# Performance work log

Measured on AMD Instinct MI355X. Metric: run time of the kernel, lower is better.

Reference implementation:

```python
import jax, jax.numpy as jnp
import numpy as np

QMIN, QMAX = -128, 127  # 8-bit signed quantized range


def setup_inputs() -> dict:
    key = jax.random.key(0)
    k0, k1, k2, k3 = jax.random.split(key, 4)
    N, Cin, H, W = 64, 128, 56, 56
    Cout, K = 128, 3
    x = jax.random.randint(k0, (N, Cin, H, W), -128, 128, dtype=jnp.int32).astype(jnp.int8)
    weight = jax.random.randint(k1, (Cout, Cin, K, K), -128, 128, dtype=jnp.int32).astype(jnp.int8)
    # int32 bias (already shifted by -Zx*sum(W) in the original quantization flow)
    bias = jax.random.randint(k2, (Cout,), -4096, 4096, dtype=jnp.int32)
    input_scale = jnp.float32(0.02)
    weight_scale = jax.random.uniform(k3, (Cout,), minval=0.001, maxval=0.01, dtype=jnp.float32)  # per-channel
    output_scale = jnp.float32(0.05)
    input_zero_point = -3   # python int, constant
    output_zero_point = -2  # python int, constant
    return {"x": x, "weight": weight, "bias": bias,
            "input_scale": input_scale, "weight_scale": weight_scale,
            "output_scale": output_scale,
            "input_zero_point": input_zero_point,
            "output_zero_point": output_zero_point}


def reference(x, weight, bias, input_scale, weight_scale, output_scale,
              input_zero_point, output_zero_point):
    # pad spatial dims with the INPUT zero point (padding=(1,1), as in the torch module)
    xp = jnp.pad(x, ((0, 0), (0, 0), (1, 1), (1, 1)), constant_values=input_zero_point)
    acc = jax.lax.conv_general_dilated(
        xp.astype(jnp.int32), weight.astype(jnp.int32),
        window_strides=(1, 1), padding='VALID',
        rhs_dilation=(1, 1), dimension_numbers=('NCHW', 'OIHW', 'NCHW'))
    acc = acc + bias[None, :, None, None]                       # [N,Co,Ho,Wo] int32
    # requantize: per-output-channel scale, shift by output zero point
    scale = (input_scale * weight_scale / output_scale)[None, :, None, None]
    out = acc.astype(jnp.float32) * scale + jnp.float32(output_zero_point)
    return jnp.clip(jnp.round(out), QMIN, QMAX).astype(jnp.int8)
```

## Files before the change

### kernel.cpp

```cpp
#include <hip/hip_runtime.h>


#define CIN  128
#define COUT 128
#define HW   56
#define NPIX (HW * HW)
#define ROWS  4
#define QROWS 6
#define QCOLS 58
#define NQ (QROWS * QCOLS)

typedef int v4i  __attribute__((ext_vector_type(4)));
typedef int v16i __attribute__((ext_vector_type(16)));

__global__ __launch_bounds__(256) void pack_w2(const int* __restrict__ w_g,
                                               unsigned* __restrict__ wp2) {
    int i = blockIdx.x * 256 + threadIdx.x;
    if (i >= 36 * 128 * 8) return;
    int dw   = i & 7;
    int cout = (i >> 3) & 127;
    int step = i >> 10;
    int t  = step >> 2;
    int cb = step & 3;
    unsigned d = 0;
#pragma unroll
    for (int b = 0; b < 4; ++b) {
        int ci = cb * 32 + dw * 4 + b;
        int v = w_g[(cout * CIN + ci) * 9 + t];
        d |= (unsigned)(v & 0xFF) << (8 * b);
    }
    int g  = (cout << 1) | (dw >> 2);
    int gs = g ^ ((g >> 3) & 7);
    wp2[step * 1024 + gs * 4 + (dw & 3)] = d;
}

__global__ __launch_bounds__(256, 2) void conv_mfma(
    const int* __restrict__ x_g, const int* __restrict__ wp2,
    const int* __restrict__ bias, const float* __restrict__ in_s,
    const float* __restrict__ w_s, const float* __restrict__ out_s,
    const int* __restrict__ zp_in_p, const int* __restrict__ zp_out_p,
    int* __restrict__ out) {
    __shared__ unsigned xs[NQ * 32];
    __shared__ char Bb[2][8192];
    __shared__ float scs[COUT];
    __shared__ int   bis[COUT];

    const int n   = blockIdx.x / 14;
    const int ho0 = (blockIdx.x % 14) * ROWS;
    const int tid    = threadIdx.x;
    const int lane   = tid & 63;
    const int wave   = tid >> 6;
    const int lane31 = lane & 31;
    const int hi     = lane >> 5;
    const int hi4    = hi * 4;

    const unsigned zpd = (unsigned)((*zp_in_p) & 0xFF) * 0x01010101u;

    if (tid < COUT) {
        scs[tid] = ((*in_s) / (*out_s)) * w_s[tid];
        bis[tid] = bias[tid];
    }

#pragma unroll
    for (int it = 0; it < 2; ++it) {
        int idx = it * 256 + tid;
        if (idx < QROWS * 2 * 32) {
            int ci4 = idx & 31;
            int r   = idx >> 6;
            int q   = r * QCOLS + (((idx >> 5) & 1) ? QCOLS - 1 : 0);
            xs[q * 32 + (ci4 ^ ((q & 7) << 2))] = zpd;
        }
    }
    if (ho0 == 0 || ho0 == HW - ROWS) {
        int rpad = (ho0 == 0) ? 0 : QROWS - 1;
#pragma unroll
        for (int it = 0; it < 7; ++it) {
            int idx = it * 256 + tid;
            int c   = idx % HW + 1;
            int ci4 = idx / HW;
            int q   = rpad * QCOLS + c;
            xs[q * 32 + (ci4 ^ ((q & 7) << 2))] = zpd;
        }
    }
#pragma unroll
    for (int it = 0; it < 11; ++it) {
        int tau = it * 256 + tid;
        if (tau < QROWS * 14 * 32) {
            int cg   = tau % 14;
            int rest = tau / 14;
            int ci4  = rest & 31;
            int r    = rest >> 5;
            int h = ho0 + r - 1;
            if ((unsigned)h < HW) {
                const int* xb = x_g + ((n * CIN + ci4 * 4) * HW + h) * HW + cg * 4;
                v4i L0 = *(const v4i*)xb;
                v4i L1 = *(const v4i*)(xb + NPIX);
                v4i L2 = *(const v4i*)(xb + 2 * NPIX);
                v4i L3 = *(const v4i*)(xb + 3 * NPIX);
#pragma unroll
                for (int j = 0; j < 4; ++j) {
                    unsigned d = (unsigned)(L0[j] & 0xFF) |
                                 ((unsigned)(L1[j] & 0xFF) << 8) |
                                 ((unsigned)(L2[j] & 0xFF) << 16) |
                                 ((unsigned)(L3[j] & 0xFF) << 24);
                    int q = r * QCOLS + cg * 4 + 1 + j;
                    xs[q * 32 + (ci4 ^ ((q & 7) << 2))] = d;
                }
            }
        }
    }
    {
        const char* gsrc = (const char*)wp2 + tid * 16;
        v4i r0 = *(const v4i*)gsrc;
        v4i r1 = *(const v4i*)(gsrc + 4096);
        *(v4i*)(&Bb[0][tid * 16])        = r0;
        *(v4i*)(&Bb[0][4096 + tid * 16]) = r1;
    }
    __syncthreads();

    int qb[2];
#pragma unroll
    for (int i = 0; i < 2; ++i) {
        int px = (wave * 2 + i) * 32 + lane31;
        if (px > ROWS * HW - 1) px = ROWS * HW - 1;
        qb[i] = (px / HW) * QCOLS + (px % HW);
    }
    int boff[4];
#pragma unroll
    for (int nt = 0; nt < 4; ++nt) {
        int g = nt * 64 + lane31 * 2 + hi;
        boff[nt] = (g ^ ((g >> 3) & 7)) * 16;
    }

    v16i acc[2][4];
#pragma unroll
    for (int i = 0; i < 2; ++i)
#pragma unroll
        for (int j = 0; j < 4; ++j) acc[i][j] = (v16i)0;

#pragma unroll 1
    for (int u = 0; u < 18; ++u) {
        v4i r0, r1;
        if (u < 17) {
            const char* gsrc = (const char*)wp2 + (u + 1) * 8192 + tid * 16;
            r0 = *(const v4i*)gsrc;
            r1 = *(const v4i*)(gsrc + 4096);
        }
        const int t  = u >> 1;
        const int dq = (t / 3) * QCOLS + (t % 3);
        const int q0 = qb[0] + dq, q1 = qb[1] + dq;
        const int s0 = (q0 & 7) << 2, s1 = (q1 & 7) << 2;
        const char* bb = Bb[u & 1];
#pragma unroll
        for (int c = 0; c < 2; ++c) {
            const int cb = (u & 1) * 2 + c;
            v4i a0 = *(const v4i*)&xs[q0 * 32 + ((cb * 8 + hi4) ^ s0)];
            v4i a1 = *(const v4i*)&xs[q1 * 32 + ((cb * 8 + hi4) ^ s1)];
            const char* bc = bb + c * 4096;
            v4i b0 = *(const v4i*)(bc + boff[0]);
            v4i b1 = *(const v4i*)(bc + boff[1]);
            v4i b2 = *(const v4i*)(bc + boff[2]);
            v4i b3 = *(const v4i*)(bc + boff[3]);
            acc[0][0] = __builtin_amdgcn_mfma_i32_32x32x32_i8(b0, a0, acc[0][0], 0, 0, 0);
            acc[0][1] = __builtin_amdgcn_mfma_i32_32x32x32_i8(b1, a0, acc[0][1], 0, 0, 0);
            acc[0][2] = __builtin_amdgcn_mfma_i32_32x32x32_i8(b2, a0, acc[0][2], 0, 0, 0);
            acc[0][3] = __builtin_amdgcn_mfma_i32_32x32x32_i8(b3, a0, acc[0][3], 0, 0, 0);
            acc[1][0] = __builtin_amdgcn_mfma_i32_32x32x32_i8(b0, a1, acc[1][0], 0, 0, 0);
            acc[1][1] = __builtin_amdgcn_mfma_i32_32x32x32_i8(b1, a1, acc[1][1], 0, 0, 0);
            acc[1][2] = __builtin_amdgcn_mfma_i32_32x32x32_i8(b2, a1, acc[1][2], 0, 0, 0);
            acc[1][3] = __builtin_amdgcn_mfma_i32_32x32x32_i8(b3, a1, acc[1][3], 0, 0, 0);
        }
        if (u < 17) {
            char* ld = &Bb[(u + 1) & 1][tid * 16];
            *(v4i*)ld          = r0;
            *(v4i*)(ld + 4096) = r1;
            __syncthreads();
        }
    }

    const float zpo = (float)(*zp_out_p);
#pragma unroll
    for (int i = 0; i < 2; ++i) {
        const int px = (wave * 2 + i) * 32 + lane31;
        if (px < ROWS * HW) {
            int* ob = out + n * COUT * NPIX + ho0 * HW + px;
#pragma unroll
            for (int nt = 0; nt < 4; ++nt) {
#pragma unroll
                for (int reg = 0; reg < 16; ++reg) {
                    int co = nt * 32 + (reg & 3) + 8 * (reg >> 2) + hi4;
                    float f = fmaf((float)(acc[i][nt][reg] + bis[co]), scs[co], zpo);
                    f = rintf(f);
                    f = fminf(fmaxf(f, -128.0f), 127.0f);
                    ob[co * NPIX] = (int)f;
                }
            }
        }
    }
}

extern "C" void kernel_launch(void* const* d_in, const int* in_sizes, int n_in,
                              void* d_out, int out_size, void* d_ws, size_t ws_size,
                              hipStream_t stream) {
    const int* x_g      = (const int*)d_in[0];
    const int* w_g      = (const int*)d_in[1];
    const int* bias     = (const int*)d_in[2];
    const float* in_s   = (const float*)d_in[3];
    const float* w_s    = (const float*)d_in[4];
    const float* out_s  = (const float*)d_in[5];
    const int* zp_in_p  = (const int*)d_in[6];
    const int* zp_out_p = (const int*)d_in[7];
    int* outp = (int*)d_out;
    unsigned* wp2 = (unsigned*)d_ws;

    pack_w2<<<(36 * 128 * 8 + 255) / 256, 256, 0, stream>>>(w_g, wp2);

    const int nblocks = 64 * (HW / ROWS);
    conv_mfma<<<nblocks, 256, 0, stream>>>(x_g, (const int*)wp2, bias,
                                           in_s, w_s, out_s, zp_in_p, zp_out_p, outp);
}
```

Baseline: 76.48 us.

## Pre-pack padded int8 NHWC input and load tiles via global_load_lds

Adds a repack_x kernel that converts the int32 NCHW input into a padded int8 channel-packed layout in workspace, halo and zero-point padding included. The conv kernel then fills its LDS input window and weight double buffer with direct global-to-LDS 16-byte loads, using a swizzle that matches the existing read pattern. This removes per-block packing and padding logic and the register staging of weights. The cost is an extra full pass over the input. That pass uses scalar, poorly coalesced loads and adds another kernel launch.

```diff
diff --git a/kernel.cpp b/kernel.cpp
--- a/kernel.cpp
+++ b/kernel.cpp
@@ -6,12 +6,19 @@
 #define HW   56
 #define NPIX (HW * HW)
 #define ROWS  4
-#define QROWS 6
 #define QCOLS 58
-#define NQ (QROWS * QCOLS)
+#define XROW  (QCOLS * CIN)
+#define XP_OFF 147456
+#define XP_ROWS (64 * QCOLS)
 
 typedef int v4i  __attribute__((ext_vector_type(4)));
 typedef int v16i __attribute__((ext_vector_type(16)));
+
+__device__ __forceinline__ void gl16(const void* g, void* l) {
+    __builtin_amdgcn_global_load_lds(
+        (const __attribute__((address_space(1))) unsigned*)g,
+        (__attribute__((address_space(3))) unsigned*)l, 16, 0, 0);
+}
 
 __global__ __launch_bounds__(256) void pack_w2(const int* __restrict__ w_g,
                                                unsigned* __restrict__ wp2) {
@@ -34,14 +41,42 @@
     wp2[step * 1024 + gs * 4 + (dw & 3)] = d;
 }
 
+__global__ __launch_bounds__(256) void repack_x(const int* __restrict__ x_g,
+                                                unsigned char* __restrict__ xp,
+                                                const int* __restrict__ zp_in_p) {
+    const int blk = blockIdx.x;
+    const int n  = blk / QCOLS;
+    const int hp = blk % QCOLS;
+    const unsigned zpd = (unsigned)((*zp_in_p) & 0xFF) * 0x01010101u;
+    unsigned* row = (unsigned*)(xp + (size_t)blk * XROW);
+
+    if (hp == 0 || hp == QCOLS - 1) {
+        for (int d = threadIdx.x; d < QCOLS * 32; d += 256) row[d] = zpd;
+        return;
+    }
+    const int h = hp - 1;
+    for (int d = threadIdx.x; d < QCOLS * 32; d += 256) {
+        int wp  = d >> 5;
+        int ci4 = d & 31;
+        unsigned v = zpd;
+        if (wp >= 1 && wp <= HW) {
+            const int* xb = x_g + ((n * CIN + ci4 * 4) * HW + h) * HW + (wp - 1);
+            v = (unsigned)(xb[0] & 0xFF) |
+                ((unsigned)(xb[NPIX] & 0xFF) << 8) |
+                ((unsigned)(xb[2 * NPIX] & 0xFF) << 16) |
+                ((unsigned)(xb[3 * NPIX] & 0xFF) << 24);
+        }
+        row[d] = v;
+    }
+}
+
 __global__ __launch_bounds__(256, 2) void conv_mfma(
-    const int* __restrict__ x_g, const int* __restrict__ wp2,
+    const unsigned char* __restrict__ xp, const unsigned char* __restrict__ wp2b,
     const int* __restrict__ bias, const float* __restrict__ in_s,
     const float* __restrict__ w_s, const float* __restrict__ out_s,
-    const int* __restrict__ zp_in_p, const int* __restrict__ zp_out_p,
-    int* __restrict__ out) {
-    __shared__ unsigned xs[NQ * 32];
-    __shared__ char Bb[2][8192];
+    const int* __restrict__ zp_out_p, int* __restrict__ out) {
+    __shared__ unsigned char xsb[45056];
+    __shared__ unsigned char Bb2[2][8192];
     __shared__ float scs[COUT];
     __shared__ int   bis[COUT];
 
@@ -54,70 +89,27 @@
     const int hi     = lane >> 5;
     const int hi4    = hi * 4;
 
-    const unsigned zpd = (unsigned)((*zp_in_p) & 0xFF) * 0x01010101u;
-
     if (tid < COUT) {
         scs[tid] = ((*in_s) / (*out_s)) * w_s[tid];
         bis[tid] = bias[tid];
     }
 
-#pragma unroll
-    for (int it = 0; it < 2; ++it) {
-        int idx = it * 256 + tid;
-        if (idx < QROWS * 2 * 32) {
-            int ci4 = idx & 31;
-            int r   = idx >> 6;
-            int q   = r * QCOLS + (((idx >> 5) & 1) ? QCOLS - 1 : 0);
-            xs[q * 32 + (ci4 ^ ((q & 7) << 2))] = zpd;
-        }
-    }
-    if (ho0 == 0 || ho0 == HW - ROWS) {
-        int rpad = (ho0 == 0) ? 0 : QROWS - 1;
-#pragma unroll
-        for (int it = 0; it < 7; ++it) {
-            int idx = it * 256 + tid;
-            int c   = idx % HW + 1;
-            int ci4 = idx / HW;
-            int q   = rpad * QCOLS + c;
-            xs[q * 32 + (ci4 ^ ((q & 7) << 2))] = zpd;
-        }
-    }
-#pragma unroll
-    for (int it = 0; it < 11; ++it) {
-        int tau = it * 256 + tid;
-        if (tau < QROWS * 14 * 32) {
-            int cg   = tau % 14;
-            int rest = tau / 14;
-            int ci4  = rest & 31;
-            int r    = rest >> 5;
-            int h = ho0 + r - 1;
-            if ((unsigned)h < HW) {
-                const int* xb = x_g + ((n * CIN + ci4 * 4) * HW + h) * HW + cg * 4;
-                v4i L0 = *(const v4i*)xb;
-                v4i L1 = *(const v4i*)(xb + NPIX);
-                v4i L2 = *(const v4i*)(xb + 2 * NPIX);
-                v4i L3 = *(const v4i*)(xb + 3 * NPIX);
-#pragma unroll
-                for (int j = 0; j < 4; ++j) {
-                    unsigned d = (unsigned)(L0[j] & 0xFF) |
-                                 ((unsigned)(L1[j] & 0xFF) << 8) |
-                                 ((unsigned)(L2[j] & 0xFF) << 16) |
-                                 ((unsigned)(L3[j] & 0xFF) << 24);
-                    int q = r * QCOLS + cg * 4 + 1 + j;
-                    xs[q * 32 + (ci4 ^ ((q & 7) << 2))] = d;
-                }
-            }
-        }
+    const unsigned char* win = xp + (size_t)(n * QCOLS + ho0) * XROW;
+    const int qrel = lane >> 3;
+    const int lof  = (qrel * 8 + ((lane & 7) ^ qrel)) * 16;
+    for (int i = wave; i < 44; i += 4) {
+        int off = i * 1024 + lof;
+        if (i == 43 && qrel >= 4) off = lof & 0;
+        gl16(win + off, xsb + i * 1024);
     }
     {
-        const char* gsrc = (const char*)wp2 + tid * 16;
-        v4i r0 = *(const v4i*)gsrc;
-        v4i r1 = *(const v4i*)(gsrc + 4096);
-        *(v4i*)(&Bb[0][tid * 16])        = r0;
-        *(v4i*)(&Bb[0][4096 + tid * 16]) = r1;
+        const unsigned char* bs = wp2b + wave * 2048 + lane * 16;
+        gl16(bs, &Bb2[0][wave * 2048]);
+        gl16(bs + 1024, &Bb2[0][wave * 2048 + 1024]);
     }
     __syncthreads();
 
+    const unsigned* xs = (const unsigned*)xsb;
     int qb[2];
 #pragma unroll
     for (int i = 0; i < 2; ++i) {
@@ -140,23 +132,23 @@
 
 #pragma unroll 1
     for (int u = 0; u < 18; ++u) {
-        v4i r0, r1;
         if (u < 17) {
-            const char* gsrc = (const char*)wp2 + (u + 1) * 8192 + tid * 16;
-            r0 = *(const v4i*)gsrc;
-            r1 = *(const v4i*)(gsrc + 4096);
+            const unsigned char* bs = wp2b + (u + 1) * 8192 + wave * 2048 + lane * 16;
+            unsigned char* bd = &Bb2[(u + 1) & 1][wave * 2048];
+            gl16(bs, bd);
+            gl16(bs + 1024, bd + 1024);
         }
         const int t  = u >> 1;
         const int dq = (t / 3) * QCOLS + (t % 3);
         const int q0 = qb[0] + dq, q1 = qb[1] + dq;
         const int s0 = (q0 & 7) << 2, s1 = (q1 & 7) << 2;
-        const char* bb = Bb[u & 1];
+        const unsigned char* bb = Bb2[u & 1];
 #pragma unroll
         for (int c = 0; c < 2; ++c) {
             const int cb = (u & 1) * 2 + c;
             v4i a0 = *(const v4i*)&xs[q0 * 32 + ((cb * 8 + hi4) ^ s0)];
             v4i a1 = *(const v4i*)&xs[q1 * 32 + ((cb * 8 + hi4) ^ s1)];
-            const char* bc = bb + c * 4096;
+            const unsigned char* bc = bb + c * 4096;
             v4i b0 = *(const v4i*)(bc + boff[0]);
             v4i b1 = *(const v4i*)(bc + boff[1]);
             v4i b2 = *(const v4i*)(bc + boff[2]);
@@ -170,12 +162,7 @@
             acc[1][2] = __builtin_amdgcn_mfma_i32_32x32x32_i8(b2, a1, acc[1][2], 0, 0, 0);
             acc[1][3] = __builtin_amdgcn_mfma_i32_32x32x32_i8(b3, a1, acc[1][3], 0, 0, 0);
         }
-        if (u < 17) {
-            char* ld = &Bb[(u + 1) & 1][tid * 16];
-            *(v4i*)ld          = r0;
-            *(v4i*)(ld + 4096) = r1;
-            __syncthreads();
-        }
+        __syncthreads();
     }
 
     const float zpo = (float)(*zp_out_p);
@@ -212,10 +199,12 @@
     const int* zp_out_p = (const int*)d_in[7];
     int* outp = (int*)d_out;
     unsigned* wp2 = (unsigned*)d_ws;
+    unsigned char* xpp = (unsigned char*)d_ws + XP_OFF;
 
     pack_w2<<<(36 * 128 * 8 + 255) / 256, 256, 0, stream>>>(w_g, wp2);
+    repack_x<<<XP_ROWS, 256, 0, stream>>>(x_g, xpp, zp_in_p);
 
     const int nblocks = 64 * (HW / ROWS);
-    conv_mfma<<<nblocks, 256, 0, stream>>>(x_g, (const int*)wp2, bias,
-                                           in_s, w_s, out_s, zp_in_p, zp_out_p, outp);
-}
+    conv_mfma<<<nblocks, 256, 0, stream>>>(xpp, (const unsigned char*)wp2, bias,
+                                           in_s, w_s, out_s, zp_out_p, outp);
+}
```

Result: slower. 126.5 us (+65.4%).
